# Kernel optimization log

Measured on AMD Instinct MI355X. Metric: run time of the kernel, lower is better.

Reference implementation:

```python
import jax, jax.numpy as jnp
import numpy as np

B, S, E = 32, 2048, 1024   # batch, seq_len, embed_dim
R = 512                    # reasoning_dim
STEPS = 8                  # max_reasoning_steps


def setup_inputs() -> dict:
    key = jax.random.key(0)
    ks = jax.random.split(key, 6)
    inv_sqrt_r = 1.0 / np.sqrt(R)
    return {
        "x": jax.random.normal(ks[0], (B, S, E), jnp.float32),
        # BitNetLinear params init: randn * 0.1, zero bias
        "enc_W": jax.random.normal(ks[1], (R, E), jnp.float32) * 0.1,
        "enc_b": jnp.zeros((R,), jnp.float32),
        # nn.LSTM params (uniform(-1/sqrt(R), 1/sqrt(R)) in torch; normal*scale ok for ref)
        "W_ih": jax.random.normal(ks[2], (4 * R, R), jnp.float32) * inv_sqrt_r,
        "W_hh": jax.random.normal(ks[3], (4 * R, R), jnp.float32) * inv_sqrt_r,
        "b_ih": jnp.zeros((4 * R,), jnp.float32),
        "b_hh": jnp.zeros((4 * R,), jnp.float32),
        "dec_W": jax.random.normal(ks[4], (E, R), jnp.float32) * 0.1,
        "dec_b": jnp.zeros((E,), jnp.float32),
        "gate_W": jax.random.normal(ks[5], (1, R), jnp.float32) * 0.1,
        "gate_b": jnp.zeros((1,), jnp.float32),
    }


def bit_linear(x, W, b):
    """Eval-mode BitNetLinear: ternary weights {-1,0,+1}, int8 activations."""
    w_scale = jnp.mean(jnp.abs(W))
    q_w = jnp.sign(W) * (jnp.abs(W) > 0.5 * w_scale).astype(W.dtype)
    i_scale = jnp.max(jnp.abs(x)) / 127.0
    q_x = jnp.clip(jnp.round(x / i_scale), -128.0, 127.0)
    return (q_x @ q_w.T) * w_scale * i_scale + b


def reference(x, enc_W, enc_b, W_ih, W_hh, b_ih, b_hh, dec_W, dec_b, gate_W, gate_b):
    # reasoning_input = encoder(mean over seq)  -> [B, R]
    cur = bit_linear(jnp.mean(x, axis=1), enc_W, enc_b)
    h = jnp.zeros_like(cur)
    c = jnp.zeros_like(cur)
    active = jnp.array(True)  # whether loop is still running (torch break emulation)
    outs, weights = [], []
    for step in range(STEPS):
        gates = cur @ W_ih.T + h @ W_hh.T + (b_ih + b_hh)  # [B, 4R]
        i, f, g, o = jnp.split(gates, 4, axis=-1)          # torch order: i, f, g, o
        c = jax.nn.sigmoid(f) * c + jax.nn.sigmoid(i) * jnp.tanh(g)
        h = jax.nn.sigmoid(o) * jnp.tanh(c)
        outs.append(h)
        weights.append(active)
        gate_score = jax.nn.sigmoid(bit_linear(h, gate_W, gate_b))  # [B, 1]
        trigger = jnp.all(gate_score < 0.5) & (step > 2)
        active = active & jnp.logical_not(trigger)
        cur = h
    outs = jnp.stack(outs, axis=0)                                  # [T, B, R]
    w = jnp.stack(weights, axis=0).astype(x.dtype)                  # [T]
    final = jnp.einsum('t,tbr->br', w, outs) / jnp.sum(w)           # masked mean over steps
    reasoning_out = bit_linear(final, dec_W, dec_b)                 # [B, E]
    return x + reasoning_out[:, None, :]                            # broadcast over seq
```

## Files before the change

### kernel.cpp

```cpp
#include <hip/hip_runtime.h>
#include <math.h>

#define NB 32
#define NS 2048
#define NE 1024
#define NR 512
#define FR 2048
#define NSTEPS 8

#define SCAL   ((size_t)0)
#define PART   ((size_t)1024)
#define WB_IH  (PART + (size_t)NB*32*NE)
#define WB_SUM (WB_IH + (size_t)FR*NR/2)
#define MEANB  (WB_SUM + (size_t)FR*NR/2)
#define HBUF   (MEANB + (size_t)NB*NE)
#define HBUFB  (HBUF + (size_t)9*NB*NR)
#define CBUF   (HBUFB + (size_t)9*NB*NR/2)
#define FINALB (CBUF + (size_t)NB*NR)
#define ROUTB  (FINALB + (size_t)NB*NR)
#define LOGIT  (SCAL + 64)

typedef __attribute__((ext_vector_type(8))) short bf16x8;
typedef __attribute__((ext_vector_type(4))) float f32x4;

__device__ __forceinline__ float sigf(float x){ return 1.0f/(1.0f+expf(-x)); }
__device__ __forceinline__ float quant8(float x, float isc){
    return fminf(fmaxf(rintf(x/isc), -128.0f), 127.0f);
}
__device__ __forceinline__ float tern(float w, float thr){
    return (fabsf(w) > thr) ? (w > 0.0f ? 1.0f : -1.0f) : 0.0f;
}
__device__ __forceinline__ unsigned short f2b(float x){
    unsigned u = __float_as_uint(x);
    return (unsigned short)((u + 0x7fffu + ((u >> 16) & 1u)) >> 16);
}

__global__ __launch_bounds__(256) void k_pre(
    const float4* __restrict__ x4, const float* __restrict__ Wih,
    const float* __restrict__ Whh, const float* __restrict__ encW,
    const float* __restrict__ decW, const float* __restrict__ gateW,
    float* __restrict__ ws)
{
    const int blk = blockIdx.x, tid = threadIdx.x;
    if (blk < 1024) {
        const int b = blk >> 5, ch = blk & 31;
        const float4* xp = x4 + ((size_t)(b*NS + ch*64))*(NE/4) + tid;
        float4 a; a.x=0.f; a.y=0.f; a.z=0.f; a.w=0.f;
        #pragma unroll 4
        for (int i = 0; i < 64; i++) {
            float4 v = xp[(size_t)i*(NE/4)];
            a.x += v.x; a.y += v.y; a.z += v.z; a.w += v.w;
        }
        float4* pp = (float4*)(ws + PART) + (size_t)blk*(NE/4) + tid;
        *pp = a;
    } else if (blk < 1152) {
        const int lb = blk - 1024;
        const float4* wih4 = (const float4*)Wih;
        const float4* whh4 = (const float4*)Whh;
        ushort4* bi = (ushort4*)(ws + WB_IH);
        ushort4* bs = (ushort4*)(ws + WB_SUM);
        #pragma unroll
        for (int i = 0; i < 8; i++) {
            const int idx = lb*256 + tid + i*32768;
            float4 a = wih4[idx];
            float4 c = whh4[idx];
            ushort4 va; va.x=f2b(a.x); va.y=f2b(a.y); va.z=f2b(a.z); va.w=f2b(a.w);
            ushort4 vs; vs.x=f2b(a.x+c.x); vs.y=f2b(a.y+c.y); vs.z=f2b(a.z+c.z); vs.w=f2b(a.w+c.w);
            bi[idx] = va; bs[idx] = vs;
        }
    } else {
        const float4* w4; int n4; int lb; float* dst;
        if (blk < 1216)      { w4=(const float4*)encW;  n4=NR*NE/4; lb=blk-1152; dst=ws+SCAL+0; }
        else if (blk < 1280) { w4=(const float4*)decW;  n4=NE*NR/4; lb=blk-1216; dst=ws+SCAL+1; }
        else                 { w4=(const float4*)gateW; n4=NR/4;    lb=0;        dst=ws+SCAL+2; }
        float a = 0.f;
        for (int i = lb*256 + tid; i < n4; i += 64*256) {
            float4 v = w4[i];
            a += fabsf(v.x)+fabsf(v.y)+fabsf(v.z)+fabsf(v.w);
        }
        for (int o = 32; o > 0; o >>= 1) a += __shfl_down(a, o, 64);
        __shared__ float lds[4];
        if ((tid & 63) == 0) lds[tid >> 6] = a;
        __syncthreads();
        if (tid == 0) atomicAdd(dst, lds[0]+lds[1]+lds[2]+lds[3]);
    }
}

__global__ __launch_bounds__(256) void k_mean(float* __restrict__ ws)
{
    const int b = blockIdx.x, tid = threadIdx.x;
    const float4* pp = (const float4*)(ws + PART) + (size_t)b*32*(NE/4);
    float4 a; a.x=0.f; a.y=0.f; a.z=0.f; a.w=0.f;
    #pragma unroll 4
    for (int c = 0; c < 32; c++) {
        float4 v = pp[(size_t)c*(NE/4) + tid];
        a.x += v.x; a.y += v.y; a.z += v.z; a.w += v.w;
    }
    const float inv = 1.0f/(float)NS;
    a.x *= inv; a.y *= inv; a.z *= inv; a.w *= inv;
    ((float4*)(ws + MEANB))[(size_t)b*(NE/4) + tid] = a;
    float m = fmaxf(fmaxf(fabsf(a.x), fabsf(a.y)), fmaxf(fabsf(a.z), fabsf(a.w)));
    for (int o = 32; o > 0; o >>= 1) m = fmaxf(m, __shfl_down(m, o, 64));
    __shared__ float lds[4];
    if ((tid & 63) == 0) lds[tid >> 6] = m;
    __syncthreads();
    if (tid == 0) {
        m = fmaxf(fmaxf(lds[0], lds[1]), fmaxf(lds[2], lds[3]));
        atomicMax((unsigned int*)(ws + SCAL + 4), __float_as_uint(m));
    }
}

__global__ __launch_bounds__(256) void k_enc(
    const float* __restrict__ encW, const float* __restrict__ encB,
    float* __restrict__ ws)
{
    const int blk = blockIdx.x, tid = threadIdx.x;
    const int b = blk >> 1;
    const int r = ((blk & 1) << 8) + tid;
    const float wsc = ws[SCAL+0] * (1.0f/(float)(NR*NE));
    const float thr = 0.5f*wsc;
    const float amax = __uint_as_float(((const unsigned int*)(ws + SCAL))[4]);
    const float isc = amax / 127.0f;
    __shared__ float qx[NE];
    const float* mrow = ws + MEANB + (size_t)b*NE;
    for (int e = tid; e < NE; e += 256) qx[e] = quant8(mrow[e], isc);
    __syncthreads();
    const float4* w4 = (const float4*)(encW + (size_t)r*NE);
    float acc = 0.f;
    #pragma unroll 4
    for (int e = 0; e < NE; e += 4) {
        float4 w = w4[e >> 2];
        acc += qx[e  ]*tern(w.x, thr) + qx[e+1]*tern(w.y, thr)
             + qx[e+2]*tern(w.z, thr) + qx[e+3]*tern(w.w, thr);
    }
    const float h0 = acc*wsc*isc + encB[r];
    ws[HBUF + (size_t)b*NR + r] = h0;
    ((unsigned short*)(ws + HBUFB))[(size_t)b*NR + r] = f2b(h0);
    ws[CBUF + (size_t)b*NR + r] = 0.f;
}

__global__ __launch_bounds__(256) void k_step(
    const unsigned short* __restrict__ wb,
    const float* __restrict__ bih, const float* __restrict__ bhh,
    float* __restrict__ ws, int t)
{
    const int tid = threadIdx.x;
    const int wv = tid >> 6, lane = tid & 63;
    const int n = lane & 15, quad = lane >> 4;
    const int mt = blockIdx.x & 1;
    const int r0 = (blockIdx.x >> 1) << 4;
    const unsigned short* hb = (const unsigned short*)(ws + HBUFB) + (size_t)t*NB*NR;
    const unsigned short* ap = hb + (size_t)(mt*16 + n)*NR + quad*8;
    const unsigned short* bp = wb + (size_t)((wv << 9) + r0 + n)*NR + quad*8;
    f32x4 acc = {0.f, 0.f, 0.f, 0.f};
    #pragma unroll
    for (int k0 = 0; k0 < NR; k0 += 32) {
        bf16x8 af = *(const bf16x8*)(ap + k0);
        bf16x8 bf_ = *(const bf16x8*)(bp + k0);
        acc = __builtin_amdgcn_mfma_f32_16x16x32_bf16(af, bf_, acc, 0, 0, 0);
    }
    __shared__ float g[4][16][17];
    #pragma unroll
    for (int reg = 0; reg < 4; reg++)
        g[wv][quad*4 + reg][n] = acc[reg];
    __syncthreads();
    const int bl = tid >> 4, rl = tid & 15;
    const int r = r0 + rl, b = mt*16 + bl;
    const float gi = g[0][bl][rl] + bih[r]        + bhh[r];
    const float gf = g[1][bl][rl] + bih[NR+r]     + bhh[NR+r];
    const float gg = g[2][bl][rl] + bih[2*NR+r]   + bhh[2*NR+r];
    const float go = g[3][bl][rl] + bih[3*NR+r]   + bhh[3*NR+r];
    const float c  = ws[CBUF + (size_t)b*NR + r];
    const float cn = sigf(gf)*c + sigf(gi)*tanhf(gg);
    const float hn = sigf(go)*tanhf(cn);
    ws[CBUF + (size_t)b*NR + r] = cn;
    ws[HBUF + (size_t)(t+1)*NB*NR + (size_t)b*NR + r] = hn;
    ((unsigned short*)(ws + HBUFB))[(size_t)(t+1)*NB*NR + (size_t)b*NR + r] = f2b(hn);
    float m = fabsf(hn);
    for (int o = 32; o > 0; o >>= 1) m = fmaxf(m, __shfl_down(m, o, 64));
    __shared__ float red[4];
    if (lane == 0) red[wv] = m;
    __syncthreads();
    if (tid == 0) {
        m = fmaxf(fmaxf(red[0], red[1]), fmaxf(red[2], red[3]));
        atomicMax((unsigned int*)(ws + SCAL + 8 + t), __float_as_uint(m));
    }
}

__global__ __launch_bounds__(256) void k_glog(
    const float* __restrict__ gateW, const float* __restrict__ gateB,
    float* __restrict__ ws)
{
    const int t = blockIdx.x, tid = threadIdx.x;
    __shared__ float qgw[NR];
    __shared__ float lp[256];
    const float gwsc = ws[SCAL+2] * (1.0f/(float)NR);
    const float gthr = 0.5f*gwsc;
    for (int i = tid; i < NR; i += 256) qgw[i] = tern(gateW[i], gthr);
    __syncthreads();
    const float amax = __uint_as_float(((const unsigned int*)(ws + SCAL))[8 + t]);
    const float isc = amax / 127.0f;
    const float* h = ws + HBUF + (size_t)(t+1)*NB*NR;
    const int b = tid >> 3, ch = tid & 7;
    const float* hbp = h + (size_t)b*NR + ch*64;
    float s = 0.f;
    for (int i = 0; i < 64; i++) s += quant8(hbp[i], isc) * qgw[ch*64 + i];
    lp[tid] = s;
    __syncthreads();
    if (tid < NB) {
        float z = 0.f;
        for (int c = 0; c < 8; c++) z += lp[tid*8 + c];
        ws[LOGIT + t*32 + tid] = z*gwsc*isc + gateB[0];
    }
}

__global__ __launch_bounds__(256) void k_final(float* __restrict__ ws)
{
    const int tid = threadIdx.x, blk = blockIdx.x;
    float wts[NSTEPS];
    bool active = true;
    #pragma unroll
    for (int t = 0; t < NSTEPS; t++) {
        bool allneg = true;
        for (int b = 0; b < NB; b++)
            allneg = allneg && (ws[LOGIT + t*32 + b] < 0.0f);
        const bool trig = allneg && (t > 2);
        wts[t] = active ? 1.0f : 0.0f;
        active = active && !trig;
    }
    float wsum = 0.f;
    #pragma unroll
    for (int t = 0; t < NSTEPS; t++) wsum += wts[t];
    const float inv = 1.0f/wsum;
    float m = 0.f;
    const int i0 = blk*512 + tid;
    #pragma unroll
    for (int rep = 0; rep < 2; rep++) {
        const int i = i0 + rep*256;
        float f = 0.f;
        #pragma unroll
        for (int t = 0; t < NSTEPS; t++)
            f += wts[t]*ws[HBUF + (size_t)(t+1)*NB*NR + i];
        f *= inv;
        ws[FINALB + i] = f;
        m = fmaxf(m, fabsf(f));
    }
    for (int o = 32; o > 0; o >>= 1) m = fmaxf(m, __shfl_down(m, o, 64));
    __shared__ float red[4];
    if ((tid & 63) == 0) red[tid >> 6] = m;
    __syncthreads();
    if (tid == 0) {
        m = fmaxf(fmaxf(red[0], red[1]), fmaxf(red[2], red[3]));
        atomicMax((unsigned int*)(ws + SCAL + 5), __float_as_uint(m));
    }
}

__global__ __launch_bounds__(256) void k_dec(
    const float* __restrict__ decW, const float* __restrict__ decB,
    float* __restrict__ ws)
{
    const int blk = blockIdx.x, tid = threadIdx.x;
    const int b = blk >> 2;
    const int e = ((blk & 3) << 8) + tid;
    const float wsc = ws[SCAL+1] * (1.0f/(float)(NE*NR));
    const float thr = 0.5f*wsc;
    const float isc = __uint_as_float(((const unsigned int*)(ws + SCAL))[5]) / 127.0f;
    __shared__ float qf[NR];
    const float* frow = ws + FINALB + (size_t)b*NR;
    for (int i = tid; i < NR; i += 256) qf[i] = quant8(frow[i], isc);
    __syncthreads();
    const float4* w4 = (const float4*)(decW + (size_t)e*NR);
    float acc = 0.f;
    #pragma unroll 4
    for (int r = 0; r < NR; r += 4) {
        float4 w = w4[r >> 2];
        acc += qf[r  ]*tern(w.x, thr) + qf[r+1]*tern(w.y, thr)
             + qf[r+2]*tern(w.z, thr) + qf[r+3]*tern(w.w, thr);
    }
    ws[ROUTB + (size_t)b*NE + e] = acc*wsc*isc + decB[e];
}

__global__ __launch_bounds__(256) void k_out(
    const float4* __restrict__ x4, const float* __restrict__ ws,
    float4* __restrict__ out4)
{
    const float4* r4 = (const float4*)(ws + ROUTB);
    const size_t base = (size_t)blockIdx.x*1024 + threadIdx.x;
    #pragma unroll
    for (int i = 0; i < 4; i++) {
        size_t f = base + (size_t)i*256;
        int e4 = (int)(f & 255);
        int b  = (int)(f >> 19);
        float4 xv = x4[f];
        float4 rv = r4[(size_t)b*256 + e4];
        float4 o; o.x = xv.x+rv.x; o.y = xv.y+rv.y; o.z = xv.z+rv.z; o.w = xv.w+rv.w;
        out4[f] = o;
    }
}

extern "C" void kernel_launch(void* const* d_in, const int* in_sizes, int n_in,
                              void* d_out, int out_size, void* d_ws, size_t ws_size,
                              hipStream_t stream)
{
    const float* x     = (const float*)d_in[0];
    const float* encW  = (const float*)d_in[1];
    const float* encB  = (const float*)d_in[2];
    const float* Wih   = (const float*)d_in[3];
    const float* Whh   = (const float*)d_in[4];
    const float* bih   = (const float*)d_in[5];
    const float* bhh   = (const float*)d_in[6];
    const float* decW  = (const float*)d_in[7];
    const float* decB  = (const float*)d_in[8];
    const float* gateW = (const float*)d_in[9];
    const float* gateB = (const float*)d_in[10];
    float* ws  = (float*)d_ws;
    float* out = (float*)d_out;

    hipMemsetAsync(d_ws, 0, 4096, stream);

    hipLaunchKernelGGL(k_pre, dim3(1281), dim3(256), 0, stream,
                       (const float4*)x, Wih, Whh, encW, decW, gateW, ws);
    hipLaunchKernelGGL(k_mean, dim3(32), dim3(256), 0, stream, ws);
    hipLaunchKernelGGL(k_enc, dim3(64), dim3(256), 0, stream, encW, encB, ws);
    for (int t = 0; t < NSTEPS; t++) {
        const unsigned short* wb =
            (const unsigned short*)(ws + (t == 0 ? WB_IH : WB_SUM));
        hipLaunchKernelGGL(k_step, dim3(64), dim3(256), 0, stream, wb, bih, bhh, ws, t);
    }
    hipLaunchKernelGGL(k_glog, dim3(8), dim3(256), 0, stream, gateW, gateB, ws);
    hipLaunchKernelGGL(k_final, dim3(32), dim3(256), 0, stream, ws);
    hipLaunchKernelGGL(k_dec, dim3(128), dim3(256), 0, stream, decW, decB, ws);
    hipLaunchKernelGGL(k_out, dim3(16384), dim3(256), 0, stream,
                       (const float4*)x, ws, (float4*)out);
}
```

Measured before the change: 643.2 us.

## Fuse encoder, LSTM steps, gating and decoder into one persistent kernel

Merges the mean, encoder, eight LSTM step kernels, gate logits, final averaging and decoder into a single 64-block persistent kernel. Stages are separated by a software grid barrier built on atomics in the workspace, replacing about a dozen small launches. The encoder and decoder matvecs now pre-ternarize weights to bf16 and run on MFMA. Risks are barrier spin overhead and correctness that depends on all 64 blocks being co-resident. The overall time is dominated by the x read and output write, so the gain is limited to launch overhead.

```diff
diff --git a/kernel.cpp b/kernel.cpp
--- a/kernel.cpp
+++ b/kernel.cpp
@@ -7,6 +7,7 @@
 #define NR 512
 #define FR 2048
 #define NSTEPS 8
+#define MID_BLOCKS 64
 
 #define SCAL   ((size_t)0)
 #define PART   ((size_t)1024)
@@ -18,6 +19,8 @@
 #define CBUF   (HBUFB + (size_t)9*NB*NR/2)
 #define FINALB (CBUF + (size_t)NB*NR)
 #define ROUTB  (FINALB + (size_t)NB*NR)
+#define ENCWB  (ROUTB + (size_t)NB*NE)
+#define DECWB  (ENCWB + (size_t)NR*NE/2)
 #define LOGIT  (SCAL + 64)
 
 typedef __attribute__((ext_vector_type(8))) short bf16x8;
@@ -33,6 +36,24 @@
 __device__ __forceinline__ unsigned short f2b(float x){
     unsigned u = __float_as_uint(x);
     return (unsigned short)((u + 0x7fffu + ((u >> 16) & 1u)) >> 16);
+}
+
+__device__ __forceinline__ void gridbar(unsigned* bar) {
+    __syncthreads();
+    if (threadIdx.x == 0) {
+        __threadfence();
+        unsigned g = __hip_atomic_fetch_add(bar+1, 0u, __ATOMIC_RELAXED, __HIP_MEMORY_SCOPE_AGENT);
+        unsigned a = __hip_atomic_fetch_add(bar,   1u, __ATOMIC_ACQ_REL, __HIP_MEMORY_SCOPE_AGENT);
+        if (a == (unsigned)(MID_BLOCKS - 1)) {
+            (void)__hip_atomic_exchange(bar, 0u, __ATOMIC_RELAXED, __HIP_MEMORY_SCOPE_AGENT);
+            (void)__hip_atomic_fetch_add(bar+1, 1u, __ATOMIC_ACQ_REL, __HIP_MEMORY_SCOPE_AGENT);
+        } else {
+            while (__hip_atomic_fetch_add(bar+1, 0u, __ATOMIC_RELAXED, __HIP_MEMORY_SCOPE_AGENT) == g)
+                __builtin_amdgcn_s_sleep(4);
+        }
+        __threadfence();
+    }
+    __syncthreads();
 }
 
 __global__ __launch_bounds__(256) void k_pre(
@@ -86,198 +107,225 @@
     }
 }
 
-__global__ __launch_bounds__(256) void k_mean(float* __restrict__ ws)
-{
-    const int b = blockIdx.x, tid = threadIdx.x;
-    const float4* pp = (const float4*)(ws + PART) + (size_t)b*32*(NE/4);
-    float4 a; a.x=0.f; a.y=0.f; a.z=0.f; a.w=0.f;
-    #pragma unroll 4
-    for (int c = 0; c < 32; c++) {
-        float4 v = pp[(size_t)c*(NE/4) + tid];
-        a.x += v.x; a.y += v.y; a.z += v.z; a.w += v.w;
-    }
-    const float inv = 1.0f/(float)NS;
-    a.x *= inv; a.y *= inv; a.z *= inv; a.w *= inv;
-    ((float4*)(ws + MEANB))[(size_t)b*(NE/4) + tid] = a;
-    float m = fmaxf(fmaxf(fabsf(a.x), fabsf(a.y)), fmaxf(fabsf(a.z), fabsf(a.w)));
-    for (int o = 32; o > 0; o >>= 1) m = fmaxf(m, __shfl_down(m, o, 64));
-    __shared__ float lds[4];
-    if ((tid & 63) == 0) lds[tid >> 6] = m;
-    __syncthreads();
-    if (tid == 0) {
-        m = fmaxf(fmaxf(lds[0], lds[1]), fmaxf(lds[2], lds[3]));
-        atomicMax((unsigned int*)(ws + SCAL + 4), __float_as_uint(m));
-    }
-}
-
-__global__ __launch_bounds__(256) void k_enc(
+__global__ __launch_bounds__(256, 1) void k_mid(
     const float* __restrict__ encW, const float* __restrict__ encB,
+    const float* __restrict__ decW, const float* __restrict__ decB,
+    const float* __restrict__ gateW, const float* __restrict__ gateB,
+    const float* __restrict__ bih, const float* __restrict__ bhh,
     float* __restrict__ ws)
 {
-    const int blk = blockIdx.x, tid = threadIdx.x;
-    const int b = blk >> 1;
-    const int r = ((blk & 1) << 8) + tid;
-    const float wsc = ws[SCAL+0] * (1.0f/(float)(NR*NE));
-    const float thr = 0.5f*wsc;
-    const float amax = __uint_as_float(((const unsigned int*)(ws + SCAL))[4]);
-    const float isc = amax / 127.0f;
-    __shared__ float qx[NE];
-    const float* mrow = ws + MEANB + (size_t)b*NE;
-    for (int e = tid; e < NE; e += 256) qx[e] = quant8(mrow[e], isc);
-    __syncthreads();
-    const float4* w4 = (const float4*)(encW + (size_t)r*NE);
-    float acc = 0.f;
-    #pragma unroll 4
-    for (int e = 0; e < NE; e += 4) {
-        float4 w = w4[e >> 2];
-        acc += qx[e  ]*tern(w.x, thr) + qx[e+1]*tern(w.y, thr)
-             + qx[e+2]*tern(w.z, thr) + qx[e+3]*tern(w.w, thr);
-    }
-    const float h0 = acc*wsc*isc + encB[r];
-    ws[HBUF + (size_t)b*NR + r] = h0;
-    ((unsigned short*)(ws + HBUFB))[(size_t)b*NR + r] = f2b(h0);
-    ws[CBUF + (size_t)b*NR + r] = 0.f;
-}
-
-__global__ __launch_bounds__(256) void k_step(
-    const unsigned short* __restrict__ wb,
-    const float* __restrict__ bih, const float* __restrict__ bhh,
-    float* __restrict__ ws, int t)
-{
-    const int tid = threadIdx.x;
+    const int bid = blockIdx.x, tid = threadIdx.x;
     const int wv = tid >> 6, lane = tid & 63;
     const int n = lane & 15, quad = lane >> 4;
-    const int mt = blockIdx.x & 1;
-    const int r0 = (blockIdx.x >> 1) << 4;
-    const unsigned short* hb = (const unsigned short*)(ws + HBUFB) + (size_t)t*NB*NR;
-    const unsigned short* ap = hb + (size_t)(mt*16 + n)*NR + quad*8;
-    const unsigned short* bp = wb + (size_t)((wv << 9) + r0 + n)*NR + quad*8;
-    f32x4 acc = {0.f, 0.f, 0.f, 0.f};
-    #pragma unroll
-    for (int k0 = 0; k0 < NR; k0 += 32) {
-        bf16x8 af = *(const bf16x8*)(ap + k0);
-        bf16x8 bf_ = *(const bf16x8*)(bp + k0);
-        acc = __builtin_amdgcn_mfma_f32_16x16x32_bf16(af, bf_, acc, 0, 0, 0);
-    }
-    __shared__ float g[4][16][17];
-    #pragma unroll
-    for (int reg = 0; reg < 4; reg++)
-        g[wv][quad*4 + reg][n] = acc[reg];
-    __syncthreads();
-    const int bl = tid >> 4, rl = tid & 15;
-    const int r = r0 + rl, b = mt*16 + bl;
-    const float gi = g[0][bl][rl] + bih[r]        + bhh[r];
-    const float gf = g[1][bl][rl] + bih[NR+r]     + bhh[NR+r];
-    const float gg = g[2][bl][rl] + bih[2*NR+r]   + bhh[2*NR+r];
-    const float go = g[3][bl][rl] + bih[3*NR+r]   + bhh[3*NR+r];
-    const float c  = ws[CBUF + (size_t)b*NR + r];
-    const float cn = sigf(gf)*c + sigf(gi)*tanhf(gg);
-    const float hn = sigf(go)*tanhf(cn);
-    ws[CBUF + (size_t)b*NR + r] = cn;
-    ws[HBUF + (size_t)(t+1)*NB*NR + (size_t)b*NR + r] = hn;
-    ((unsigned short*)(ws + HBUFB))[(size_t)(t+1)*NB*NR + (size_t)b*NR + r] = f2b(hn);
-    float m = fabsf(hn);
-    for (int o = 32; o > 0; o >>= 1) m = fmaxf(m, __shfl_down(m, o, 64));
-    __shared__ float red[4];
-    if (lane == 0) red[wv] = m;
-    __syncthreads();
-    if (tid == 0) {
-        m = fmaxf(fmaxf(red[0], red[1]), fmaxf(red[2], red[3]));
-        atomicMax((unsigned int*)(ws + SCAL + 8 + t), __float_as_uint(m));
-    }
-}
-
-__global__ __launch_bounds__(256) void k_glog(
-    const float* __restrict__ gateW, const float* __restrict__ gateB,
-    float* __restrict__ ws)
-{
-    const int t = blockIdx.x, tid = threadIdx.x;
-    __shared__ float qgw[NR];
-    __shared__ float lp[256];
-    const float gwsc = ws[SCAL+2] * (1.0f/(float)NR);
-    const float gthr = 0.5f*gwsc;
-    for (int i = tid; i < NR; i += 256) qgw[i] = tern(gateW[i], gthr);
-    __syncthreads();
-    const float amax = __uint_as_float(((const unsigned int*)(ws + SCAL))[8 + t]);
-    const float isc = amax / 127.0f;
-    const float* h = ws + HBUF + (size_t)(t+1)*NB*NR;
-    const int b = tid >> 3, ch = tid & 7;
-    const float* hbp = h + (size_t)b*NR + ch*64;
-    float s = 0.f;
-    for (int i = 0; i < 64; i++) s += quant8(hbp[i], isc) * qgw[ch*64 + i];
-    lp[tid] = s;
-    __syncthreads();
-    if (tid < NB) {
-        float z = 0.f;
-        for (int c = 0; c < 8; c++) z += lp[tid*8 + c];
-        ws[LOGIT + t*32 + tid] = z*gwsc*isc + gateB[0];
-    }
-}
-
-__global__ __launch_bounds__(256) void k_final(float* __restrict__ ws)
-{
-    const int tid = threadIdx.x, blk = blockIdx.x;
-    float wts[NSTEPS];
-    bool active = true;
-    #pragma unroll
+    unsigned* bar = (unsigned*)ws + 1020;
+
+    __shared__ float sG[4][16][17];
+    __shared__ float sRed[4];
+    __shared__ float sQgw[NR];
+    __shared__ float sLp[256];
+    __shared__ int sAllneg[NSTEPS];
+
+    if (bid < 32) {
+        const float4* pp = (const float4*)(ws + PART) + (size_t)bid*32*(NE/4);
+        float4 a; a.x=0.f; a.y=0.f; a.z=0.f; a.w=0.f;
+        #pragma unroll 4
+        for (int c = 0; c < 32; c++) {
+            float4 v = pp[(size_t)c*(NE/4) + tid];
+            a.x += v.x; a.y += v.y; a.z += v.z; a.w += v.w;
+        }
+        const float inv = 1.0f/(float)NS;
+        a.x *= inv; a.y *= inv; a.z *= inv; a.w *= inv;
+        ((float4*)(ws + MEANB))[(size_t)bid*(NE/4) + tid] = a;
+        float m = fmaxf(fmaxf(fabsf(a.x), fabsf(a.y)), fmaxf(fabsf(a.z), fabsf(a.w)));
+        for (int o = 32; o > 0; o >>= 1) m = fmaxf(m, __shfl_down(m, o, 64));
+        if (lane == 0) sRed[wv] = m;
+        __syncthreads();
+        if (tid == 0) {
+            m = fmaxf(fmaxf(sRed[0], sRed[1]), fmaxf(sRed[2], sRed[3]));
+            atomicMax((unsigned int*)(ws + SCAL) + 4, __float_as_uint(m));
+        }
+    } else {
+        const int lb = bid - 32;
+        const float* W; const float* scal; ushort4* dst; int base;
+        if (lb < 16) { W = encW; scal = ws+SCAL+0; dst = (ushort4*)(ws+ENCWB); base = lb; }
+        else         { W = decW; scal = ws+SCAL+1; dst = (ushort4*)(ws+DECWB); base = lb-16; }
+        const float wsc = *scal * (1.0f/(float)(NR*NE));
+        const float thr = 0.5f*wsc;
+        const float4* w4 = (const float4*)W;
+        #pragma unroll 4
+        for (int i = 0; i < 32; i++) {
+            const int idx = base*8192 + i*256 + tid;
+            float4 w = w4[idx];
+            ushort4 v;
+            v.x = f2b(tern(w.x, thr)); v.y = f2b(tern(w.y, thr));
+            v.z = f2b(tern(w.z, thr)); v.w = f2b(tern(w.w, thr));
+            dst[idx] = v;
+        }
+    }
+    gridbar(bar);
+
+    {
+        const int mt = bid & 1, r0 = (bid >> 1) << 4;
+        const float amax = __uint_as_float(((const unsigned int*)(ws + SCAL))[4]);
+        const float isc = amax * (1.0f/127.0f);
+        const float wsc = ws[SCAL+0] * (1.0f/(float)(NR*NE));
+        const float* arow = ws + MEANB + (size_t)(mt*16 + n)*NE + wv*256 + quad*8;
+        const unsigned short* bp = (const unsigned short*)(ws + ENCWB)
+                                   + (size_t)(r0 + n)*NE + wv*256 + quad*8;
+        f32x4 acc = {0.f, 0.f, 0.f, 0.f};
+        #pragma unroll
+        for (int k0 = 0; k0 < 256; k0 += 32) {
+            float4 a0 = *(const float4*)(arow + k0);
+            float4 a1 = *(const float4*)(arow + k0 + 4);
+            bf16x8 af;
+            af[0]=(short)f2b(quant8(a0.x,isc)); af[1]=(short)f2b(quant8(a0.y,isc));
+            af[2]=(short)f2b(quant8(a0.z,isc)); af[3]=(short)f2b(quant8(a0.w,isc));
+            af[4]=(short)f2b(quant8(a1.x,isc)); af[5]=(short)f2b(quant8(a1.y,isc));
+            af[6]=(short)f2b(quant8(a1.z,isc)); af[7]=(short)f2b(quant8(a1.w,isc));
+            bf16x8 bf_ = *(const bf16x8*)(bp + k0);
+            acc = __builtin_amdgcn_mfma_f32_16x16x32_bf16(af, bf_, acc, 0, 0, 0);
+        }
+        #pragma unroll
+        for (int reg = 0; reg < 4; reg++) sG[wv][quad*4 + reg][n] = acc[reg];
+        __syncthreads();
+        const int bl = tid >> 4, rl = tid & 15;
+        const float v = sG[0][bl][rl] + sG[1][bl][rl] + sG[2][bl][rl] + sG[3][bl][rl];
+        const int b = mt*16 + bl, r = r0 + rl;
+        const float h0 = v*wsc*isc + encB[r];
+        ws[HBUF + (size_t)b*NR + r] = h0;
+        ((unsigned short*)(ws + HBUFB))[(size_t)b*NR + r] = f2b(h0);
+        ws[CBUF + (size_t)b*NR + r] = 0.f;
+    }
+    gridbar(bar);
+
+    #pragma unroll 1
     for (int t = 0; t < NSTEPS; t++) {
-        bool allneg = true;
-        for (int b = 0; b < NB; b++)
-            allneg = allneg && (ws[LOGIT + t*32 + b] < 0.0f);
-        const bool trig = allneg && (t > 2);
-        wts[t] = active ? 1.0f : 0.0f;
-        active = active && !trig;
-    }
-    float wsum = 0.f;
-    #pragma unroll
-    for (int t = 0; t < NSTEPS; t++) wsum += wts[t];
-    const float inv = 1.0f/wsum;
-    float m = 0.f;
-    const int i0 = blk*512 + tid;
-    #pragma unroll
-    for (int rep = 0; rep < 2; rep++) {
-        const int i = i0 + rep*256;
+        const unsigned short* wb = (const unsigned short*)(ws + (t == 0 ? WB_IH : WB_SUM));
+        const int mt = bid & 1, r0 = (bid >> 1) << 4;
+        const unsigned short* hb = (const unsigned short*)(ws + HBUFB) + (size_t)t*NB*NR;
+        const unsigned short* ap = hb + (size_t)(mt*16 + n)*NR + quad*8;
+        const unsigned short* bp = wb + (size_t)((wv << 9) + r0 + n)*NR + quad*8;
+        f32x4 acc = {0.f, 0.f, 0.f, 0.f};
+        #pragma unroll
+        for (int k0 = 0; k0 < NR; k0 += 32) {
+            bf16x8 af = *(const bf16x8*)(ap + k0);
+            bf16x8 bf_ = *(const bf16x8*)(bp + k0);
+            acc = __builtin_amdgcn_mfma_f32_16x16x32_bf16(af, bf_, acc, 0, 0, 0);
+        }
+        __syncthreads();
+        #pragma unroll
+        for (int reg = 0; reg < 4; reg++) sG[wv][quad*4 + reg][n] = acc[reg];
+        __syncthreads();
+        const int bl = tid >> 4, rl = tid & 15;
+        const int r = r0 + rl, b = mt*16 + bl;
+        const float gi = sG[0][bl][rl] + bih[r]        + bhh[r];
+        const float gf = sG[1][bl][rl] + bih[NR+r]     + bhh[NR+r];
+        const float gg = sG[2][bl][rl] + bih[2*NR+r]   + bhh[2*NR+r];
+        const float go = sG[3][bl][rl] + bih[3*NR+r]   + bhh[3*NR+r];
+        const float c  = ws[CBUF + (size_t)b*NR + r];
+        const float cn = sigf(gf)*c + sigf(gi)*tanhf(gg);
+        const float hn = sigf(go)*tanhf(cn);
+        ws[CBUF + (size_t)b*NR + r] = cn;
+        ws[HBUF + (size_t)(t+1)*NB*NR + (size_t)b*NR + r] = hn;
+        ((unsigned short*)(ws + HBUFB))[(size_t)(t+1)*NB*NR + (size_t)b*NR + r] = f2b(hn);
+        float m = fabsf(hn);
+        for (int o = 32; o > 0; o >>= 1) m = fmaxf(m, __shfl_down(m, o, 64));
+        if (lane == 0) sRed[wv] = m;
+        __syncthreads();
+        if (tid == 0) {
+            m = fmaxf(fmaxf(sRed[0], sRed[1]), fmaxf(sRed[2], sRed[3]));
+            atomicMax((unsigned int*)(ws + SCAL) + (8 + t), __float_as_uint(m));
+        }
+        gridbar(bar);
+    }
+
+    if (bid < NSTEPS) {
+        const int t = bid;
+        const float gwsc = ws[SCAL+2] * (1.0f/(float)NR);
+        const float gthr = 0.5f*gwsc;
+        for (int i = tid; i < NR; i += 256) sQgw[i] = tern(gateW[i], gthr);
+        __syncthreads();
+        const float amax = __uint_as_float(((const unsigned int*)(ws + SCAL))[8 + t]);
+        const float isc = amax * (1.0f/127.0f);
+        const float* h = ws + HBUF + (size_t)(t+1)*NB*NR;
+        const int b = tid >> 3, ch = tid & 7;
+        const float* hbp = h + (size_t)b*NR + ch*64;
+        float s = 0.f;
+        for (int i = 0; i < 64; i++) s += quant8(hbp[i], isc) * sQgw[ch*64 + i];
+        sLp[tid] = s;
+        __syncthreads();
+        if (tid < NB) {
+            float z = 0.f;
+            for (int c2 = 0; c2 < 8; c2++) z += sLp[tid*8 + c2];
+            ws[LOGIT + t*32 + tid] = z*gwsc*isc + gateB[0];
+        }
+    }
+    gridbar(bar);
+
+    {
+        if (tid < NSTEPS) {
+            int an = 1;
+            for (int b = 0; b < NB; b++)
+                an &= (ws[LOGIT + tid*32 + b] < 0.0f) ? 1 : 0;
+            sAllneg[tid] = an;
+        }
+        __syncthreads();
+        float wts[NSTEPS]; bool active = true; float wsum = 0.f;
+        #pragma unroll
+        for (int t = 0; t < NSTEPS; t++) {
+            const bool trig = (sAllneg[t] != 0) && (t > 2);
+            wts[t] = active ? 1.0f : 0.0f;
+            wsum += wts[t];
+            active = active && !trig;
+        }
+        const float inv = 1.0f/wsum;
+        const int i = bid*256 + tid;
         float f = 0.f;
         #pragma unroll
         for (int t = 0; t < NSTEPS; t++)
             f += wts[t]*ws[HBUF + (size_t)(t+1)*NB*NR + i];
         f *= inv;
         ws[FINALB + i] = f;
-        m = fmaxf(m, fabsf(f));
-    }
-    for (int o = 32; o > 0; o >>= 1) m = fmaxf(m, __shfl_down(m, o, 64));
-    __shared__ float red[4];
-    if ((tid & 63) == 0) red[tid >> 6] = m;
-    __syncthreads();
-    if (tid == 0) {
-        m = fmaxf(fmaxf(red[0], red[1]), fmaxf(red[2], red[3]));
-        atomicMax((unsigned int*)(ws + SCAL + 5), __float_as_uint(m));
-    }
-}
-
-__global__ __launch_bounds__(256) void k_dec(
-    const float* __restrict__ decW, const float* __restrict__ decB,
-    float* __restrict__ ws)
-{
-    const int blk = blockIdx.x, tid = threadIdx.x;
-    const int b = blk >> 2;
-    const int e = ((blk & 3) << 8) + tid;
-    const float wsc = ws[SCAL+1] * (1.0f/(float)(NE*NR));
-    const float thr = 0.5f*wsc;
-    const float isc = __uint_as_float(((const unsigned int*)(ws + SCAL))[5]) / 127.0f;
-    __shared__ float qf[NR];
-    const float* frow = ws + FINALB + (size_t)b*NR;
-    for (int i = tid; i < NR; i += 256) qf[i] = quant8(frow[i], isc);
-    __syncthreads();
-    const float4* w4 = (const float4*)(decW + (size_t)e*NR);
-    float acc = 0.f;
-    #pragma unroll 4
-    for (int r = 0; r < NR; r += 4) {
-        float4 w = w4[r >> 2];
-        acc += qf[r  ]*tern(w.x, thr) + qf[r+1]*tern(w.y, thr)
-             + qf[r+2]*tern(w.z, thr) + qf[r+3]*tern(w.w, thr);
-    }
-    ws[ROUTB + (size_t)b*NE + e] = acc*wsc*isc + decB[e];
+        float m = fabsf(f);
+        for (int o = 32; o > 0; o >>= 1) m = fmaxf(m, __shfl_down(m, o, 64));
+        if (lane == 0) sRed[wv] = m;
+        __syncthreads();
+        if (tid == 0) {
+            m = fmaxf(fmaxf(sRed[0], sRed[1]), fmaxf(sRed[2], sRed[3]));
+            atomicMax((unsigned int*)(ws + SCAL) + 5, __float_as_uint(m));
+        }
+    }
+    gridbar(bar);
+
+    {
+        const int mt = bid & 1, gp = bid >> 1;
+        if (wv < 2) {
+            const int e0 = (gp*2 + wv) << 4;
+            const float isc = __uint_as_float(((const unsigned int*)(ws + SCAL))[5]) * (1.0f/127.0f);
+            const float wsc = ws[SCAL+1] * (1.0f/(float)(NE*NR));
+            const float* arow = ws + FINALB + (size_t)(mt*16 + n)*NR + quad*8;
+            const unsigned short* bp = (const unsigned short*)(ws + DECWB)
+                                       + (size_t)(e0 + n)*NR + quad*8;
+            f32x4 acc = {0.f, 0.f, 0.f, 0.f};
+            #pragma unroll
+            for (int k0 = 0; k0 < NR; k0 += 32) {
+                float4 a0 = *(const float4*)(arow + k0);
+                float4 a1 = *(const float4*)(arow + k0 + 4);
+                bf16x8 af;
+                af[0]=(short)f2b(quant8(a0.x,isc)); af[1]=(short)f2b(quant8(a0.y,isc));
+                af[2]=(short)f2b(quant8(a0.z,isc)); af[3]=(short)f2b(quant8(a0.w,isc));
+                af[4]=(short)f2b(quant8(a1.x,isc)); af[5]=(short)f2b(quant8(a1.y,isc));
+                af[6]=(short)f2b(quant8(a1.z,isc)); af[7]=(short)f2b(quant8(a1.w,isc));
+                bf16x8 bf_ = *(const bf16x8*)(bp + k0);
+                acc = __builtin_amdgcn_mfma_f32_16x16x32_bf16(af, bf_, acc, 0, 0, 0);
+            }
+            #pragma unroll
+            for (int reg = 0; reg < 4; reg++) {
+                const int b = mt*16 + quad*4 + reg;
+                ws[ROUTB + (size_t)b*NE + e0 + n] = acc[reg]*wsc*isc + decB[e0 + n];
+            }
+        }
+    }
 }
 
 __global__ __launch_bounds__(256) void k_out(
@@ -320,16 +368,8 @@
 
     hipLaunchKernelGGL(k_pre, dim3(1281), dim3(256), 0, stream,
                        (const float4*)x, Wih, Whh, encW, decW, gateW, ws);
-    hipLaunchKernelGGL(k_mean, dim3(32), dim3(256), 0, stream, ws);
-    hipLaunchKernelGGL(k_enc, dim3(64), dim3(256), 0, stream, encW, encB, ws);
-    for (int t = 0; t < NSTEPS; t++) {
-        const unsigned short* wb =
-            (const unsigned short*)(ws + (t == 0 ? WB_IH : WB_SUM));
-        hipLaunchKernelGGL(k_step, dim3(64), dim3(256), 0, stream, wb, bih, bhh, ws, t);
-    }
-    hipLaunchKernelGGL(k_glog, dim3(8), dim3(256), 0, stream, gateW, gateB, ws);
-    hipLaunchKernelGGL(k_final, dim3(32), dim3(256), 0, stream, ws);
-    hipLaunchKernelGGL(k_dec, dim3(128), dim3(256), 0, stream, decW, decB, ws);
+    hipLaunchKernelGGL(k_mid, dim3(MID_BLOCKS), dim3(256), 0, stream,
+                       encW, encB, decW, decB, gateW, gateB, bih, bhh, ws);
     hipLaunchKernelGGL(k_out, dim3(16384), dim3(256), 0, stream,
                        (const float4*)x, ws, (float4*)out);
 }
```

Result: no change. 641.3 us (-0.3%).
